# Performance work log

Measured on AMD Instinct MI355X. Metric: run time of the kernel, lower is better.

## Reference

```python
import jax, jax.numpy as jnp
import numpy as np

N, D = 8192, 32
SIGMA = 4.0
DAMPING = 0.5
MAX_ITER = 10
SHIFT_TOL = 1e-4


def _sqdist(a, b):
    # squared euclidean distances, (Na, Nb)
    sq = jnp.sum(a * a, axis=1)[:, None] + jnp.sum(b * b, axis=1)[None, :] - 2.0 * (a @ b.T)
    return jnp.maximum(sq, 0.0)


def setup_inputs() -> dict:
    key = jax.random.key(0)
    x = jax.random.normal(key, (N, D), dtype=jnp.float32)
    sigma = jnp.asarray(SIGMA, dtype=jnp.float32)  # learned scalar nn.Parameter
    return {"x": x, "sigma": sigma}


def _find_centroids(x, sigma):
    gamma = 1.0 / (2.0 * sigma ** 2)

    def body(carry, _):
        centroids, done = carry
        sq = _sqdist(x, centroids)              # (N, N); cdist(x,c)**2
        w = jnp.exp(-sq * gamma)                # gaussian kernel weights
        new_c = (w @ x) / jnp.sum(w, axis=1, keepdims=True)
        shift = jnp.linalg.norm(new_c - centroids, axis=1)
        # torch breaks BEFORE the damping update when max shift < tol
        done_new = done | (jnp.max(shift) < SHIFT_TOL)
        centroids = jnp.where(done_new, centroids,
                              DAMPING * centroids + (1.0 - DAMPING) * new_c)
        return (centroids, done_new), None

    (centroids, _), _ = jax.lax.scan(jax.remat(body), (x, jnp.asarray(False)), None, length=MAX_ITER)
    return centroids


def _nms_keep(x, centroids, threshold):
    n = centroids.shape[0]
    sq_pc = _sqdist(x, centroids)
    closest = jnp.argmin(sq_pc, axis=1)                      # (N,)
    scores = jnp.zeros((n,), jnp.int32).at[closest].add(1)   # counts per centroid
    sq_cc = _sqdist(centroids, centroids)
    overlap = (sq_cc < threshold ** 2) & ~jnp.eye(n, dtype=bool)
    order = jnp.argsort(-scores)                             # descending by score

    def body(keep, idx):
        active = keep[idx]
        keep2 = jnp.where(active, keep & ~overlap[idx], keep)
        keep2 = keep2.at[idx].set(jnp.where(active, scores[idx] > 0, keep2[idx]))
        return keep2, None

    keep, _ = jax.lax.scan(body, jnp.ones((n,), bool), order)
    return keep


def reference(x, sigma):
    centroids = _find_centroids(x, sigma)
    # threshold = sigma.item() in torch -> constant w.r.t. autodiff
    keep = _nms_keep(x, centroids, jax.lax.stop_gradient(sigma))
    # assignment over kept centroids only (dropped centroids get -inf cost -> 0 prob)
    cost = -jnp.sqrt(_sqdist(x, centroids) + 1e-12)
    cost = jnp.where(keep[None, :], cost, -jnp.inf)
    assignment = jax.nn.softmax(cost, axis=1)  # alpha == 1 branch
    return centroids, assignment, keep
```

## Files before the change

### kernel.cpp

```cpp
#include <hip/hip_runtime.h>
#include <math.h>

#define NPTS 8192
#define DIM 32
#define MAX_ITER 10
#define TOL 1e-4f
#define DAMP 0.5f
#define LOG2E 1.4426950408889634f

#define OFF_MSP   0u
#define OFF_CCUR  8650752u
#define OFF_CNEW  8912896u
#define OFF_NX    9175040u
#define OFF_NC    9183232u
#define OFF_PV    9191424u
#define OFF_PJ    9453568u
#define OFF_RKP   9715712u
#define OFF_MSH   9977856u
#define OFF_SCO   9977872u
#define OFF_ORD   9986064u

__global__ __launch_bounds__(256) void k_init(const float* __restrict__ x,
                                              float* __restrict__ c0,
                                              float* __restrict__ nx,
                                              float* __restrict__ nc,
                                              int* __restrict__ scores,
                                              unsigned int* __restrict__ msh) {
    int p = blockIdx.x * blockDim.x + threadIdx.x;
    const float4* xr = (const float4*)(x + (size_t)p * DIM);
    float4* cr = (float4*)(c0 + (size_t)p * DIM);
    float s = 0.f;
#pragma unroll
    for (int q = 0; q < 8; ++q) {
        float4 v = xr[q];
        cr[q] = v;
        s += v.x * v.x + v.y * v.y + v.z * v.z + v.w * v.w;
    }
    nx[p] = s;
    nc[p] = s;
    scores[p] = 0;
    if (blockIdx.x == 0 && threadIdx.x < 16) msh[threadIdx.x] = 0u;
}

__global__ __launch_bounds__(256, 2) void k_ms2(const float* __restrict__ x,
                                                const float* __restrict__ nx,
                                                const float* __restrict__ c,
                                                const float* __restrict__ nc,
                                                const float* __restrict__ sigma_p,
                                                float* __restrict__ P) {
    __shared__ float sc[256 * 32];
    __shared__ float sxx[128 * 32];
    __shared__ float snc[256];

    int t = threadIdx.x;
    int wv = __builtin_amdgcn_readfirstlane(t >> 6);
    int lane = t & 63;
    int it = (int)blockIdx.x >> 5, js = (int)blockIdx.x & 31;
    int i0 = it * 512 + wv * 128 + lane;
    int i1 = i0 + 64;
    int jb = js * 256;

    float sg = sigma_p[0];
    float ng2 = -LOG2E / (2.f * sg * sg);

    float xi0[DIM], xi1[DIM];
    {
        const float4* xr0 = (const float4*)(x + (size_t)i0 * DIM);
        const float4* xr1 = (const float4*)(x + (size_t)i1 * DIM);
#pragma unroll
        for (int q = 0; q < 8; ++q) {
            float4 a = xr0[q], b = xr1[q];
            xi0[4 * q] = a.x; xi0[4 * q + 1] = a.y; xi0[4 * q + 2] = a.z; xi0[4 * q + 3] = a.w;
            xi1[4 * q] = b.x; xi1[4 * q + 1] = b.y; xi1[4 * q + 2] = b.z; xi1[4 * q + 3] = b.w;
        }
    }
    float nx0 = nx[i0], nx1 = nx[i1];

    {
        const float4* srcc = (const float4*)(c + (size_t)jb * DIM);
        float4* dstc = (float4*)sc;
        for (int k = t; k < 2048; k += 256) dstc[k] = srcc[k];
        snc[t] = nc[jb + t];
        const float4* srcx = (const float4*)(x + (size_t)jb * DIM);
        float4* dstx = (float4*)sxx;
        for (int k = t; k < 1024; k += 256) dstx[k] = srcx[k];
    }
    __syncthreads();

    float acc0[DIM], acc1[DIM];
#pragma unroll
    for (int d = 0; d < DIM; ++d) { acc0[d] = 0.f; acc1[d] = 0.f; }
    float ws0 = 0.f, ws1 = 0.f;

    for (int half = 0; half < 2; ++half) {
        int jo = half * 128;
        for (int jj = 0; jj < 128; ++jj) {
            float w0, w1;
            {
                const float4* cr = (const float4*)(sc + (size_t)(jo + jj) * 32);
                float4 C[8];
#pragma unroll
                for (int q = 0; q < 8; ++q) C[q] = cr[q];
                float ncj = snc[jo + jj];
                float a0 = 0.f, a1 = 0.f, a2 = 0.f, a3 = 0.f;
                float b0 = 0.f, b1 = 0.f, b2 = 0.f, b3 = 0.f;
#pragma unroll
                for (int q = 0; q < 8; ++q) {
                    a0 = fmaf(xi0[4 * q + 0], C[q].x, a0);
                    a1 = fmaf(xi0[4 * q + 1], C[q].y, a1);
                    a2 = fmaf(xi0[4 * q + 2], C[q].z, a2);
                    a3 = fmaf(xi0[4 * q + 3], C[q].w, a3);
                    b0 = fmaf(xi1[4 * q + 0], C[q].x, b0);
                    b1 = fmaf(xi1[4 * q + 1], C[q].y, b1);
                    b2 = fmaf(xi1[4 * q + 2], C[q].z, b2);
                    b3 = fmaf(xi1[4 * q + 3], C[q].w, b3);
                }
                float sq0 = fmaxf(fmaf(-2.f, (a0 + a1) + (a2 + a3), nx0 + ncj), 0.f);
                float sq1 = fmaxf(fmaf(-2.f, (b0 + b1) + (b2 + b3), nx1 + ncj), 0.f);
                w0 = __builtin_amdgcn_exp2f(ng2 * sq0);
                w1 = __builtin_amdgcn_exp2f(ng2 * sq1);
            }
            ws0 += w0; ws1 += w1;
            {
                const float4* xr2 = (const float4*)(sxx + (size_t)jj * 32);
                float4 X[8];
#pragma unroll
                for (int q = 0; q < 8; ++q) X[q] = xr2[q];
#pragma unroll
                for (int q = 0; q < 8; ++q) {
                    acc0[4 * q + 0] = fmaf(w0, X[q].x, acc0[4 * q + 0]);
                    acc0[4 * q + 1] = fmaf(w0, X[q].y, acc0[4 * q + 1]);
                    acc0[4 * q + 2] = fmaf(w0, X[q].z, acc0[4 * q + 2]);
                    acc0[4 * q + 3] = fmaf(w0, X[q].w, acc0[4 * q + 3]);
                    acc1[4 * q + 0] = fmaf(w1, X[q].x, acc1[4 * q + 0]);
                    acc1[4 * q + 1] = fmaf(w1, X[q].y, acc1[4 * q + 1]);
                    acc1[4 * q + 2] = fmaf(w1, X[q].z, acc1[4 * q + 2]);
                    acc1[4 * q + 3] = fmaf(w1, X[q].w, acc1[4 * q + 3]);
                }
            }
        }
        if (half == 0) {
            __syncthreads();
            const float4* srcx = (const float4*)(x + (size_t)(jb + 128) * DIM);
            float4* dstx = (float4*)sxx;
            for (int k = t; k < 1024; k += 256) dstx[k] = srcx[k];
            __syncthreads();
        }
    }

    size_t base = ((size_t)js * 33) * NPTS + i0;
#pragma unroll
    for (int d = 0; d < DIM; ++d) {
        P[base + (size_t)d * NPTS] = acc0[d];
        P[base + (size_t)d * NPTS + 64] = acc1[d];
    }
    P[base + (size_t)32 * NPTS] = ws0;
    P[base + (size_t)32 * NPTS + 64] = ws1;
}

__global__ __launch_bounds__(256) void k_reduce(const float* __restrict__ P,
                                                const float* __restrict__ c_cur,
                                                float* __restrict__ c_new,
                                                unsigned int* __restrict__ maxshift) {
    int i = blockIdx.x * 256 + threadIdx.x;
    float tot[33];
#pragma unroll
    for (int d = 0; d < 33; ++d) tot[d] = 0.f;
    for (int js = 0; js < 32; ++js) {
        size_t base = ((size_t)js * 33) * NPTS + i;
#pragma unroll
        for (int d = 0; d < 33; ++d) tot[d] += P[base + (size_t)d * NPTS];
    }
    float ws = tot[32];
    float inv = __builtin_amdgcn_rcpf(ws);
    inv = inv * (2.f - ws * inv);
    const float* co = c_cur + (size_t)i * DIM;
    float sh2 = 0.f;
    float ncv[DIM];
#pragma unroll
    for (int d = 0; d < DIM; ++d) {
        float v = tot[d] * inv;
        ncv[d] = v;
        float df = v - co[d];
        sh2 = fmaf(df, df, sh2);
    }
    float4* dst = (float4*)(c_new + (size_t)i * DIM);
#pragma unroll
    for (int q = 0; q < 8; ++q)
        dst[q] = make_float4(ncv[4 * q], ncv[4 * q + 1], ncv[4 * q + 2], ncv[4 * q + 3]);
    atomicMax(maxshift, __float_as_uint(__builtin_amdgcn_sqrtf(sh2)));
}

__global__ __launch_bounds__(256) void k_update(float* __restrict__ c_cur,
                                                const float* __restrict__ c_new,
                                                float* __restrict__ nc,
                                                const unsigned int* __restrict__ maxshift) {
    if (__uint_as_float(*maxshift) < TOL) return;
    int i = blockIdx.x * 256 + threadIdx.x;
    float4* cc = (float4*)(c_cur + (size_t)i * DIM);
    const float4* cn = (const float4*)(c_new + (size_t)i * DIM);
    float s = 0.f;
#pragma unroll
    for (int q = 0; q < 8; ++q) {
        float4 a = cc[q], b = cn[q];
        float4 r = make_float4(DAMP * a.x + (1.f - DAMP) * b.x,
                               DAMP * a.y + (1.f - DAMP) * b.y,
                               DAMP * a.z + (1.f - DAMP) * b.z,
                               DAMP * a.w + (1.f - DAMP) * b.w);
        cc[q] = r;
        s += r.x * r.x + r.y * r.y + r.z * r.z + r.w * r.w;
    }
    nc[i] = s;
}

__global__ __launch_bounds__(256, 2) void k_scores2(const float* __restrict__ x,
                                                    const float* __restrict__ nx,
                                                    const float* __restrict__ c,
                                                    const float* __restrict__ nc,
                                                    float* __restrict__ pv,
                                                    int* __restrict__ pj) {
    __shared__ float sc[256 * 32];
    __shared__ float snc[256];
    int t = threadIdx.x;
    int wv = __builtin_amdgcn_readfirstlane(t >> 6);
    int lane = t & 63;
    int it = (int)blockIdx.x >> 5, js = (int)blockIdx.x & 31;
    int p0 = it * 512 + wv * 128 + lane;
    int p1 = p0 + 64;
    int jb = js * 256;

    float xi0[DIM], xi1[DIM];
    {
        const float4* xr0 = (const float4*)(x + (size_t)p0 * DIM);
        const float4* xr1 = (const float4*)(x + (size_t)p1 * DIM);
#pragma unroll
        for (int q = 0; q < 8; ++q) {
            float4 a = xr0[q], b = xr1[q];
            xi0[4 * q] = a.x; xi0[4 * q + 1] = a.y; xi0[4 * q + 2] = a.z; xi0[4 * q + 3] = a.w;
            xi1[4 * q] = b.x; xi1[4 * q + 1] = b.y; xi1[4 * q + 2] = b.z; xi1[4 * q + 3] = b.w;
        }
    }
    float nxp0 = nx[p0], nxp1 = nx[p1];

    {
        const float4* srcc = (const float4*)(c + (size_t)jb * DIM);
        float4* dstc = (float4*)sc;
        for (int k = t; k < 2048; k += 256) dstc[k] = srcc[k];
        snc[t] = nc[jb + t];
    }
    __syncthreads();

    float bv0 = INFINITY, bv1 = INFINITY;
    int bj0 = jb, bj1 = jb;
    for (int jj = 0; jj < 256; ++jj) {
        const float4* cr = (const float4*)(sc + (size_t)jj * 32);
        float4 C[8];
#pragma unroll
        for (int q = 0; q < 8; ++q) C[q] = cr[q];
        float ncj = snc[jj];
        float a0 = 0.f, a1 = 0.f, a2 = 0.f, a3 = 0.f;
        float b0 = 0.f, b1 = 0.f, b2 = 0.f, b3 = 0.f;
#pragma unroll
        for (int q = 0; q < 8; ++q) {
            a0 = fmaf(xi0[4 * q + 0], C[q].x, a0);
            a1 = fmaf(xi0[4 * q + 1], C[q].y, a1);
            a2 = fmaf(xi0[4 * q + 2], C[q].z, a2);
            a3 = fmaf(xi0[4 * q + 3], C[q].w, a3);
            b0 = fmaf(xi1[4 * q + 0], C[q].x, b0);
            b1 = fmaf(xi1[4 * q + 1], C[q].y, b1);
            b2 = fmaf(xi1[4 * q + 2], C[q].z, b2);
            b3 = fmaf(xi1[4 * q + 3], C[q].w, b3);
        }
        float sq0 = fmaxf(fmaf(-2.f, (a0 + a1) + (a2 + a3), nxp0 + ncj), 0.f);
        float sq1 = fmaxf(fmaf(-2.f, (b0 + b1) + (b2 + b3), nxp1 + ncj), 0.f);
        if (sq0 < bv0) { bv0 = sq0; bj0 = jb + jj; }
        if (sq1 < bv1) { bv1 = sq1; bj1 = jb + jj; }
    }
    pv[(size_t)js * NPTS + p0] = bv0;
    pj[(size_t)js * NPTS + p0] = bj0;
    pv[(size_t)js * NPTS + p1] = bv1;
    pj[(size_t)js * NPTS + p1] = bj1;
}

__global__ __launch_bounds__(256) void k_score_comb(const float* __restrict__ pv,
                                                    const int* __restrict__ pj,
                                                    int* __restrict__ scores) {
    int p = blockIdx.x * 256 + threadIdx.x;
    float bv = pv[p];
    int bj = pj[p];
    for (int js = 1; js < 32; ++js) {
        float v = pv[(size_t)js * NPTS + p];
        int j = pj[(size_t)js * NPTS + p];
        if (v < bv) { bv = v; bj = j; }
    }
    atomicAdd(&scores[bj], 1);
}

__global__ __launch_bounds__(256) void k_rank_part(const int* __restrict__ scores,
                                                   int* __restrict__ rkp) {
    int t = threadIdx.x;
    int wv = __builtin_amdgcn_readfirstlane(t >> 6);
    int lane = t & 63;
    int it = (int)blockIdx.x >> 5, js = (int)blockIdx.x & 31;
    int p = it * 256 + wv * 64 + lane;
    int sp = scores[p];
    int j0 = js * 256;
    int r = 0;
    for (int jj = 0; jj < 256; ++jj) {
        int sj = scores[j0 + jj];
        int j = j0 + jj;
        r += (sj > sp) || (sj == sp && j < p);
    }
    rkp[(size_t)js * NPTS + p] = r;
}

__global__ __launch_bounds__(256) void k_rank_comb(const int* __restrict__ rkp,
                                                   int* __restrict__ order) {
    int p = blockIdx.x * 256 + threadIdx.x;
    int r = 0;
    for (int js = 0; js < 32; ++js) r += rkp[(size_t)js * NPTS + p];
    order[r] = p;
}

__global__ __launch_bounds__(1024) void k_nms(const float* __restrict__ c,
                                              const int* __restrict__ order,
                                              const int* __restrict__ scores,
                                              const float* __restrict__ sigma_p,
                                              float* __restrict__ keep_out) {
    __shared__ int s_ord[NPTS];
    __shared__ unsigned char kp[NPTS];
    __shared__ int s_first[16];
    __shared__ int s_next;
    int t = threadIdx.x;
    for (int q = t; q < NPTS; q += 1024) { s_ord[q] = order[q]; kp[q] = 1; }
    __syncthreads();
    float sg = sigma_p[0];
    float thr2 = sg * sg;

    int k = 0;
    while (k < NPTS) {
        int cand = k + t;
        bool hit = (cand < NPTS) && (kp[s_ord[cand]] != 0);
        unsigned long long b = __ballot(hit);
        int wave = t >> 6;
        if ((t & 63) == 0)
            s_first[wave] = b ? (k + (wave << 6) + (__ffsll((unsigned long long)b) - 1))
                              : 0x7fffffff;
        __syncthreads();
        if (t == 0) {
            int mn = s_first[0];
            for (int w2 = 1; w2 < 16; ++w2) mn = min(mn, s_first[w2]);
            s_next = mn;
        }
        __syncthreads();
        int kf = s_next;
        if (kf == 0x7fffffff) { k += 1024; continue; }

        int idx = s_ord[kf];
        float ci[DIM];
        const float4* cr = (const float4*)(c + (size_t)idx * DIM);
#pragma unroll
        for (int q = 0; q < 8; ++q) {
            float4 v = cr[q];
            ci[4 * q] = v.x; ci[4 * q + 1] = v.y; ci[4 * q + 2] = v.z; ci[4 * q + 3] = v.w;
        }
#pragma unroll
        for (int m2 = 0; m2 < 8; ++m2) {
            int j = t + m2 * 1024;
            const float4* cj = (const float4*)(c + (size_t)j * DIM);
            float sq = 0.f;
#pragma unroll
            for (int q = 0; q < 8; ++q) {
                float4 v = cj[q];
                float e0 = v.x - ci[4 * q], e1 = v.y - ci[4 * q + 1];
                float e2 = v.z - ci[4 * q + 2], e3 = v.w - ci[4 * q + 3];
                sq += e0 * e0 + e1 * e1 + e2 * e2 + e3 * e3;
            }
            if (j != idx && sq < thr2) kp[j] = 0;
        }
        __syncthreads();
        if (t == 0) kp[idx] = (scores[idx] > 0) ? 1 : 0;
        __syncthreads();
        k = kf + 1;
    }
    __syncthreads();
    for (int q = t; q < NPTS; q += 1024) keep_out[q] = kp[q] ? 1.0f : 0.0f;
}

__global__ __launch_bounds__(256, 2) void k_apass1(const float* __restrict__ x,
                                                   const float* __restrict__ nx,
                                                   const float* __restrict__ c,
                                                   const float* __restrict__ nc,
                                                   const float* __restrict__ keepf,
                                                   float* __restrict__ ps) {
    __shared__ float sc[256 * 32];
    __shared__ float snc[256];
    __shared__ float skp[256];
    int t = threadIdx.x;
    int wv = __builtin_amdgcn_readfirstlane(t >> 6);
    int lane = t & 63;
    int it = (int)blockIdx.x >> 5, js = (int)blockIdx.x & 31;
    int p0 = it * 512 + wv * 128 + lane;
    int p1 = p0 + 64;
    int jb = js * 256;

    float xi0[DIM], xi1[DIM];
    {
        const float4* xr0 = (const float4*)(x + (size_t)p0 * DIM);
        const float4* xr1 = (const float4*)(x + (size_t)p1 * DIM);
#pragma unroll
        for (int q = 0; q < 8; ++q) {
            float4 a = xr0[q], b = xr1[q];
            xi0[4 * q] = a.x; xi0[4 * q + 1] = a.y; xi0[4 * q + 2] = a.z; xi0[4 * q + 3] = a.w;
            xi1[4 * q] = b.x; xi1[4 * q + 1] = b.y; xi1[4 * q + 2] = b.z; xi1[4 * q + 3] = b.w;
        }
    }
    float nxp0 = nx[p0], nxp1 = nx[p1];

    {
        const float4* srcc = (const float4*)(c + (size_t)jb * DIM);
        float4* dstc = (float4*)sc;
        for (int k = t; k < 2048; k += 256) dstc[k] = srcc[k];
        snc[t] = nc[jb + t];
        skp[t] = (keepf[jb + t] > 0.5f) ? 0.f : -1e38f;
    }
    __syncthreads();

    float S0 = 0.f, S1 = 0.f;
    for (int jj = 0; jj < 256; ++jj) {
        const float4* cr = (const float4*)(sc + (size_t)jj * 32);
        float4 C[8];
#pragma unroll
        for (int q = 0; q < 8; ++q) C[q] = cr[q];
        float ncj = snc[jj];
        float kadd = skp[jj];
        float a0 = 0.f, a1 = 0.f, a2 = 0.f, a3 = 0.f;
        float b0 = 0.f, b1 = 0.f, b2 = 0.f, b3 = 0.f;
#pragma unroll
        for (int q = 0; q < 8; ++q) {
            a0 = fmaf(xi0[4 * q + 0], C[q].x, a0);
            a1 = fmaf(xi0[4 * q + 1], C[q].y, a1);
            a2 = fmaf(xi0[4 * q + 2], C[q].z, a2);
            a3 = fmaf(xi0[4 * q + 3], C[q].w, a3);
            b0 = fmaf(xi1[4 * q + 0], C[q].x, b0);
            b1 = fmaf(xi1[4 * q + 1], C[q].y, b1);
            b2 = fmaf(xi1[4 * q + 2], C[q].z, b2);
            b3 = fmaf(xi1[4 * q + 3], C[q].w, b3);
        }
        float sq0 = fmaxf(fmaf(-2.f, (a0 + a1) + (a2 + a3), nxp0 + ncj), 0.f);
        float sq1 = fmaxf(fmaf(-2.f, (b0 + b1) + (b2 + b3), nxp1 + ncj), 0.f);
        float r0 = __builtin_amdgcn_sqrtf(sq0 + 1e-12f);
        float r1 = __builtin_amdgcn_sqrtf(sq1 + 1e-12f);
        S0 += __builtin_amdgcn_exp2f(fmaf(r0, -LOG2E, kadd));
        S1 += __builtin_amdgcn_exp2f(fmaf(r1, -LOG2E, kadd));
    }
    ps[(size_t)js * NPTS + p0] = S0;
    ps[(size_t)js * NPTS + p1] = S1;
}

__global__ __launch_bounds__(256, 4) void k_apass2(const float* __restrict__ x,
                                                   const float* __restrict__ c,
                                                   const float* __restrict__ keepf,
                                                   const float* __restrict__ ps,
                                                   float* __restrict__ A) {
    __shared__ float sx[128 * 36];
    __shared__ float snx[128];
    __shared__ float sscale[128];
    __shared__ float spart[256];
    int t = threadIdx.x;
    int wv = __builtin_amdgcn_readfirstlane(t >> 6);
    int lane = t & 63;
    int pt = (int)blockIdx.x >> 5, jt = (int)blockIdx.x & 31;
    int p0 = pt * 128, j0 = jt * 256;

    {
        const float4* src = (const float4*)(x + (size_t)p0 * DIM) + t * 4;
        int row = t >> 1, colh = (t & 1) * 16;
        float4* dst = (float4*)(sx + row * 36 + colh);
        float s = 0.f;
#pragma unroll
        for (int q = 0; q < 4; ++q) {
            float4 v = src[q];
            dst[q] = v;
            s += v.x * v.x + v.y * v.y + v.z * v.z + v.w * v.w;
        }
        spart[t] = s;
    }
    __syncthreads();
    if (t < 128) {
        snx[t] = spart[2 * t] + spart[2 * t + 1];
        float SS = 0.f;
        for (int js = 0; js < 32; ++js) SS += ps[(size_t)js * NPTS + p0 + t];
        sscale[t] = 1.f / SS;
    }

    int j = j0 + wv * 64 + lane;
    float cj[DIM];
    float ncj = 0.f;
    {
        const float4* cr = (const float4*)(c + (size_t)j * DIM);
#pragma unroll
        for (int q = 0; q < 8; ++q) {
            float4 v = cr[q];
            cj[4 * q] = v.x; cj[4 * q + 1] = v.y; cj[4 * q + 2] = v.z; cj[4 * q + 3] = v.w;
            ncj += v.x * v.x + v.y * v.y + v.z * v.z + v.w * v.w;
        }
    }
    float kadd = (keepf[j] > 0.5f) ? 0.f : -1e38f;
    __syncthreads();

    for (int pp = 0; pp < 128; ++pp) {
        const float4* xs = (const float4*)(sx + pp * 36);
        float d0 = 0.f, d1 = 0.f, d2 = 0.f, d3 = 0.f;
#pragma unroll
        for (int q = 0; q < 8; ++q) {
            float4 v = xs[q];
            d0 = fmaf(cj[4 * q + 0], v.x, d0);
            d1 = fmaf(cj[4 * q + 1], v.y, d1);
            d2 = fmaf(cj[4 * q + 2], v.z, d2);
            d3 = fmaf(cj[4 * q + 3], v.w, d3);
        }
        float sq = fmaxf(fmaf(-2.f, (d0 + d1) + (d2 + d3), snx[pp] + ncj), 0.f);
        float rt = __builtin_amdgcn_sqrtf(sq + 1e-12f);
        float tt = fmaf(rt, -LOG2E, kadd);
        A[(size_t)(p0 + pp) * NPTS + j] = __builtin_amdgcn_exp2f(tt) * sscale[pp];
    }
}

extern "C" void kernel_launch(void* const* d_in, const int* in_sizes, int n_in,
                              void* d_out, int out_size, void* d_ws, size_t ws_size,
                              hipStream_t stream) {
    const float* x = (const float*)d_in[0];
    const float* sigma = (const float*)d_in[1];

    float* out = (float*)d_out;
    float* OUT_C = out;
    float* A = out + (size_t)NPTS * DIM;
    float* OUT_K = A + (size_t)NPTS * NPTS;

    float* msP = A + OFF_MSP;
    float* c_cur = A + OFF_CCUR;
    float* c_new = A + OFF_CNEW;
    float* nx = A + OFF_NX;
    float* nc = A + OFF_NC;
    float* pv = A + OFF_PV;
    int* pj = (int*)(A + OFF_PJ);
    int* rkp = (int*)(A + OFF_RKP);
    unsigned int* msh = (unsigned int*)(A + OFF_MSH);
    int* scores = (int*)(A + OFF_SCO);
    int* order = (int*)(A + OFF_ORD);
    float* ps = (float*)d_ws;

    k_init<<<NPTS / 256, 256, 0, stream>>>(x, c_cur, nx, nc, scores, msh);
    for (int itr = 0; itr < MAX_ITER; ++itr) {
        k_ms2<<<512, 256, 0, stream>>>(x, nx, c_cur, nc, sigma, msP);
        k_reduce<<<NPTS / 256, 256, 0, stream>>>(msP, c_cur, c_new, msh + itr);
        k_update<<<NPTS / 256, 256, 0, stream>>>(c_cur, c_new, nc, msh + itr);
    }
    hipMemcpyAsync(OUT_C, c_cur, (size_t)NPTS * DIM * sizeof(float),
                   hipMemcpyDeviceToDevice, stream);

    k_scores2<<<512, 256, 0, stream>>>(x, nx, OUT_C, nc, pv, pj);
    k_score_comb<<<NPTS / 256, 256, 0, stream>>>(pv, pj, scores);
    k_rank_part<<<1024, 256, 0, stream>>>(scores, rkp);
    k_rank_comb<<<NPTS / 256, 256, 0, stream>>>(rkp, order);
    k_nms<<<1, 1024, 0, stream>>>(OUT_C, order, scores, sigma, OUT_K);

    k_apass1<<<512, 256, 0, stream>>>(x, nx, OUT_C, nc, OUT_K, ps);
    k_apass2<<<2048, 256, 0, stream>>>(x, OUT_C, OUT_K, ps, A);
}
```

Measured before the change: 1.987 ms.

## Split mean-shift column tiles finer, parallelize reduction, widen assignment tiles

The mean-shift partial kernel now covers 128 centroid columns per block instead of 256. That doubles the grid to 1024 blocks, halves shared memory per block, and removes the mid-loop reload and barriers. The reduction kernel splits the 64 partial slices across four wave groups and combines them in shared memory, so it runs 128 blocks instead of 32. The assignment kernel computes two columns per thread on half as many blocks, and several inner loops read shared memory directly rather than staging a row in registers. The cost is a partial buffer twice as large to write and read each iteration, plus changed occupancy hints.

```diff
diff --git a/kernel.cpp b/kernel.cpp
--- a/kernel.cpp
+++ b/kernel.cpp
@@ -9,16 +9,16 @@
 #define LOG2E 1.4426950408889634f
 
 #define OFF_MSP   0u
-#define OFF_CCUR  8650752u
-#define OFF_CNEW  8912896u
-#define OFF_NX    9175040u
-#define OFF_NC    9183232u
-#define OFF_PV    9191424u
-#define OFF_PJ    9453568u
-#define OFF_RKP   9715712u
-#define OFF_MSH   9977856u
-#define OFF_SCO   9977872u
-#define OFF_ORD   9986064u
+#define OFF_CCUR  17301504u
+#define OFF_CNEW  17563648u
+#define OFF_NX    17825792u
+#define OFF_NC    17833984u
+#define OFF_PV    17842176u
+#define OFF_PJ    18366464u
+#define OFF_RKP   18890752u
+#define OFF_MSH   19152896u
+#define OFF_SCO   19152912u
+#define OFF_ORD   19161104u
 
 __global__ __launch_bounds__(256) void k_init(const float* __restrict__ x,
                                               float* __restrict__ c0,
@@ -42,23 +42,25 @@
     if (blockIdx.x == 0 && threadIdx.x < 16) msh[threadIdx.x] = 0u;
 }
 
-__global__ __launch_bounds__(256, 2) void k_ms2(const float* __restrict__ x,
-                                                const float* __restrict__ nx,
-                                                const float* __restrict__ c,
-                                                const float* __restrict__ nc,
-                                                const float* __restrict__ sigma_p,
-                                                float* __restrict__ P) {
-    __shared__ float sc[256 * 32];
+__global__ __launch_bounds__(256)
+__attribute__((amdgpu_waves_per_eu(2, 4)))
+void k_ms2(const float* __restrict__ x,
+           const float* __restrict__ nx,
+           const float* __restrict__ c,
+           const float* __restrict__ nc,
+           const float* __restrict__ sigma_p,
+           float* __restrict__ P) {
+    __shared__ float sc[128 * 32];
     __shared__ float sxx[128 * 32];
-    __shared__ float snc[256];
+    __shared__ float snc[128];
 
     int t = threadIdx.x;
     int wv = __builtin_amdgcn_readfirstlane(t >> 6);
     int lane = t & 63;
-    int it = (int)blockIdx.x >> 5, js = (int)blockIdx.x & 31;
+    int it = (int)blockIdx.x >> 6, js = (int)blockIdx.x & 63;
     int i0 = it * 512 + wv * 128 + lane;
     int i1 = i0 + 64;
-    int jb = js * 256;
+    int jb = js * 128;
 
     float sg = sigma_p[0];
     float ng2 = -LOG2E / (2.f * sg * sg);
@@ -78,12 +80,11 @@
 
     {
         const float4* srcc = (const float4*)(c + (size_t)jb * DIM);
+        const float4* srcx = (const float4*)(x + (size_t)jb * DIM);
         float4* dstc = (float4*)sc;
-        for (int k = t; k < 2048; k += 256) dstc[k] = srcc[k];
-        snc[t] = nc[jb + t];
-        const float4* srcx = (const float4*)(x + (size_t)jb * DIM);
         float4* dstx = (float4*)sxx;
-        for (int k = t; k < 1024; k += 256) dstx[k] = srcx[k];
+        for (int k = t; k < 1024; k += 256) { dstc[k] = srcc[k]; dstx[k] = srcx[k]; }
+        if (t < 128) snc[t] = nc[jb + t];
     }
     __syncthreads();
 
@@ -92,59 +93,42 @@
     for (int d = 0; d < DIM; ++d) { acc0[d] = 0.f; acc1[d] = 0.f; }
     float ws0 = 0.f, ws1 = 0.f;
 
-    for (int half = 0; half < 2; ++half) {
-        int jo = half * 128;
-        for (int jj = 0; jj < 128; ++jj) {
-            float w0, w1;
-            {
-                const float4* cr = (const float4*)(sc + (size_t)(jo + jj) * 32);
-                float4 C[8];
-#pragma unroll
-                for (int q = 0; q < 8; ++q) C[q] = cr[q];
-                float ncj = snc[jo + jj];
-                float a0 = 0.f, a1 = 0.f, a2 = 0.f, a3 = 0.f;
-                float b0 = 0.f, b1 = 0.f, b2 = 0.f, b3 = 0.f;
-#pragma unroll
-                for (int q = 0; q < 8; ++q) {
-                    a0 = fmaf(xi0[4 * q + 0], C[q].x, a0);
-                    a1 = fmaf(xi0[4 * q + 1], C[q].y, a1);
-                    a2 = fmaf(xi0[4 * q + 2], C[q].z, a2);
-                    a3 = fmaf(xi0[4 * q + 3], C[q].w, a3);
-                    b0 = fmaf(xi1[4 * q + 0], C[q].x, b0);
-                    b1 = fmaf(xi1[4 * q + 1], C[q].y, b1);
-                    b2 = fmaf(xi1[4 * q + 2], C[q].z, b2);
-                    b3 = fmaf(xi1[4 * q + 3], C[q].w, b3);
-                }
-                float sq0 = fmaxf(fmaf(-2.f, (a0 + a1) + (a2 + a3), nx0 + ncj), 0.f);
-                float sq1 = fmaxf(fmaf(-2.f, (b0 + b1) + (b2 + b3), nx1 + ncj), 0.f);
-                w0 = __builtin_amdgcn_exp2f(ng2 * sq0);
-                w1 = __builtin_amdgcn_exp2f(ng2 * sq1);
+    for (int jj = 0; jj < 128; ++jj) {
+        int rb = jj * 32;
+        float w0, w1;
+        {
+            float a0 = 0.f, a1 = 0.f, a2 = 0.f, a3 = 0.f;
+            float b0 = 0.f, b1 = 0.f, b2 = 0.f, b3 = 0.f;
+#pragma unroll
+            for (int q = 0; q < 8; ++q) {
+                float4 cv = *(const float4*)(sc + rb + 4 * q);
+                a0 = fmaf(xi0[4 * q + 0], cv.x, a0);
+                a1 = fmaf(xi0[4 * q + 1], cv.y, a1);
+                a2 = fmaf(xi0[4 * q + 2], cv.z, a2);
+                a3 = fmaf(xi0[4 * q + 3], cv.w, a3);
+                b0 = fmaf(xi1[4 * q + 0], cv.x, b0);
+                b1 = fmaf(xi1[4 * q + 1], cv.y, b1);
+                b2 = fmaf(xi1[4 * q + 2], cv.z, b2);
+                b3 = fmaf(xi1[4 * q + 3], cv.w, b3);
             }
-            ws0 += w0; ws1 += w1;
-            {
-                const float4* xr2 = (const float4*)(sxx + (size_t)jj * 32);
-                float4 X[8];
-#pragma unroll
-                for (int q = 0; q < 8; ++q) X[q] = xr2[q];
-#pragma unroll
-                for (int q = 0; q < 8; ++q) {
-                    acc0[4 * q + 0] = fmaf(w0, X[q].x, acc0[4 * q + 0]);
-                    acc0[4 * q + 1] = fmaf(w0, X[q].y, acc0[4 * q + 1]);
-                    acc0[4 * q + 2] = fmaf(w0, X[q].z, acc0[4 * q + 2]);
-                    acc0[4 * q + 3] = fmaf(w0, X[q].w, acc0[4 * q + 3]);
-                    acc1[4 * q + 0] = fmaf(w1, X[q].x, acc1[4 * q + 0]);
-                    acc1[4 * q + 1] = fmaf(w1, X[q].y, acc1[4 * q + 1]);
-                    acc1[4 * q + 2] = fmaf(w1, X[q].z, acc1[4 * q + 2]);
-                    acc1[4 * q + 3] = fmaf(w1, X[q].w, acc1[4 * q + 3]);
-                }
-            }
-        }
-        if (half == 0) {
-            __syncthreads();
-            const float4* srcx = (const float4*)(x + (size_t)(jb + 128) * DIM);
-            float4* dstx = (float4*)sxx;
-            for (int k = t; k < 1024; k += 256) dstx[k] = srcx[k];
-            __syncthreads();
+            float ncj = snc[jj];
+            float sq0 = fmaxf(fmaf(-2.f, (a0 + a1) + (a2 + a3), nx0 + ncj), 0.f);
+            float sq1 = fmaxf(fmaf(-2.f, (b0 + b1) + (b2 + b3), nx1 + ncj), 0.f);
+            w0 = __builtin_amdgcn_exp2f(ng2 * sq0);
+            w1 = __builtin_amdgcn_exp2f(ng2 * sq1);
+        }
+        ws0 += w0; ws1 += w1;
+#pragma unroll
+        for (int q = 0; q < 8; ++q) {
+            float4 xv = *(const float4*)(sxx + rb + 4 * q);
+            acc0[4 * q + 0] = fmaf(w0, xv.x, acc0[4 * q + 0]);
+            acc0[4 * q + 1] = fmaf(w0, xv.y, acc0[4 * q + 1]);
+            acc0[4 * q + 2] = fmaf(w0, xv.z, acc0[4 * q + 2]);
+            acc0[4 * q + 3] = fmaf(w0, xv.w, acc0[4 * q + 3]);
+            acc1[4 * q + 0] = fmaf(w1, xv.x, acc1[4 * q + 0]);
+            acc1[4 * q + 1] = fmaf(w1, xv.y, acc1[4 * q + 1]);
+            acc1[4 * q + 2] = fmaf(w1, xv.z, acc1[4 * q + 2]);
+            acc1[4 * q + 3] = fmaf(w1, xv.w, acc1[4 * q + 3]);
         }
     }
 
@@ -162,33 +146,46 @@
                                                 const float* __restrict__ c_cur,
                                                 float* __restrict__ c_new,
                                                 unsigned int* __restrict__ maxshift) {
-    int i = blockIdx.x * 256 + threadIdx.x;
+    __shared__ float red[256][33];
+    int t = threadIdx.x;
+    int pl = t & 63, qs = t >> 6;
+    int i = blockIdx.x * 64 + pl;
     float tot[33];
 #pragma unroll
     for (int d = 0; d < 33; ++d) tot[d] = 0.f;
-    for (int js = 0; js < 32; ++js) {
+    for (int js = qs * 16; js < qs * 16 + 16; ++js) {
         size_t base = ((size_t)js * 33) * NPTS + i;
 #pragma unroll
         for (int d = 0; d < 33; ++d) tot[d] += P[base + (size_t)d * NPTS];
     }
-    float ws = tot[32];
-    float inv = __builtin_amdgcn_rcpf(ws);
-    inv = inv * (2.f - ws * inv);
-    const float* co = c_cur + (size_t)i * DIM;
-    float sh2 = 0.f;
-    float ncv[DIM];
-#pragma unroll
-    for (int d = 0; d < DIM; ++d) {
-        float v = tot[d] * inv;
-        ncv[d] = v;
-        float df = v - co[d];
-        sh2 = fmaf(df, df, sh2);
-    }
-    float4* dst = (float4*)(c_new + (size_t)i * DIM);
-#pragma unroll
-    for (int q = 0; q < 8; ++q)
-        dst[q] = make_float4(ncv[4 * q], ncv[4 * q + 1], ncv[4 * q + 2], ncv[4 * q + 3]);
-    atomicMax(maxshift, __float_as_uint(__builtin_amdgcn_sqrtf(sh2)));
+#pragma unroll
+    for (int d = 0; d < 33; ++d) red[t][d] = tot[d];
+    __syncthreads();
+    if (t < 64) {
+        int ii = blockIdx.x * 64 + t;
+        float tt[33];
+#pragma unroll
+        for (int d = 0; d < 33; ++d)
+            tt[d] = (red[t][d] + red[t + 64][d]) + (red[t + 128][d] + red[t + 192][d]);
+        float ws = tt[32];
+        float inv = __builtin_amdgcn_rcpf(ws);
+        inv = inv * (2.f - ws * inv);
+        const float* co = c_cur + (size_t)ii * DIM;
+        float sh2 = 0.f;
+        float ncv[DIM];
+#pragma unroll
+        for (int d = 0; d < DIM; ++d) {
+            float v = tt[d] * inv;
+            ncv[d] = v;
+            float df = v - co[d];
+            sh2 = fmaf(df, df, sh2);
+        }
+        float4* dst = (float4*)(c_new + (size_t)ii * DIM);
+#pragma unroll
+        for (int q = 0; q < 8; ++q)
+            dst[q] = make_float4(ncv[4 * q], ncv[4 * q + 1], ncv[4 * q + 2], ncv[4 * q + 3]);
+        atomicMax(maxshift, __float_as_uint(__builtin_amdgcn_sqrtf(sh2)));
+    }
 }
 
 __global__ __launch_bounds__(256) void k_update(float* __restrict__ c_cur,
@@ -253,24 +250,22 @@
     float bv0 = INFINITY, bv1 = INFINITY;
     int bj0 = jb, bj1 = jb;
     for (int jj = 0; jj < 256; ++jj) {
-        const float4* cr = (const float4*)(sc + (size_t)jj * 32);
-        float4 C[8];
-#pragma unroll
-        for (int q = 0; q < 8; ++q) C[q] = cr[q];
-        float ncj = snc[jj];
+        int rb = jj * 32;
         float a0 = 0.f, a1 = 0.f, a2 = 0.f, a3 = 0.f;
         float b0 = 0.f, b1 = 0.f, b2 = 0.f, b3 = 0.f;
 #pragma unroll
         for (int q = 0; q < 8; ++q) {
-            a0 = fmaf(xi0[4 * q + 0], C[q].x, a0);
-            a1 = fmaf(xi0[4 * q + 1], C[q].y, a1);
-            a2 = fmaf(xi0[4 * q + 2], C[q].z, a2);
-            a3 = fmaf(xi0[4 * q + 3], C[q].w, a3);
-            b0 = fmaf(xi1[4 * q + 0], C[q].x, b0);
-            b1 = fmaf(xi1[4 * q + 1], C[q].y, b1);
-            b2 = fmaf(xi1[4 * q + 2], C[q].z, b2);
-            b3 = fmaf(xi1[4 * q + 3], C[q].w, b3);
-        }
+            float4 cv = *(const float4*)(sc + rb + 4 * q);
+            a0 = fmaf(xi0[4 * q + 0], cv.x, a0);
+            a1 = fmaf(xi0[4 * q + 1], cv.y, a1);
+            a2 = fmaf(xi0[4 * q + 2], cv.z, a2);
+            a3 = fmaf(xi0[4 * q + 3], cv.w, a3);
+            b0 = fmaf(xi1[4 * q + 0], cv.x, b0);
+            b1 = fmaf(xi1[4 * q + 1], cv.y, b1);
+            b2 = fmaf(xi1[4 * q + 2], cv.z, b2);
+            b3 = fmaf(xi1[4 * q + 3], cv.w, b3);
+        }
+        float ncj = snc[jj];
         float sq0 = fmaxf(fmaf(-2.f, (a0 + a1) + (a2 + a3), nxp0 + ncj), 0.f);
         float sq1 = fmaxf(fmaf(-2.f, (b0 + b1) + (b2 + b3), nxp1 + ncj), 0.f);
         if (sq0 < bv0) { bv0 = sq0; bj0 = jb + jj; }
@@ -428,25 +423,23 @@
 
     float S0 = 0.f, S1 = 0.f;
     for (int jj = 0; jj < 256; ++jj) {
-        const float4* cr = (const float4*)(sc + (size_t)jj * 32);
-        float4 C[8];
-#pragma unroll
-        for (int q = 0; q < 8; ++q) C[q] = cr[q];
+        int rb = jj * 32;
+        float a0 = 0.f, a1 = 0.f, a2 = 0.f, a3 = 0.f;
+        float b0 = 0.f, b1 = 0.f, b2 = 0.f, b3 = 0.f;
+#pragma unroll
+        for (int q = 0; q < 8; ++q) {
+            float4 cv = *(const float4*)(sc + rb + 4 * q);
+            a0 = fmaf(xi0[4 * q + 0], cv.x, a0);
+            a1 = fmaf(xi0[4 * q + 1], cv.y, a1);
+            a2 = fmaf(xi0[4 * q + 2], cv.z, a2);
+            a3 = fmaf(xi0[4 * q + 3], cv.w, a3);
+            b0 = fmaf(xi1[4 * q + 0], cv.x, b0);
+            b1 = fmaf(xi1[4 * q + 1], cv.y, b1);
+            b2 = fmaf(xi1[4 * q + 2], cv.z, b2);
+            b3 = fmaf(xi1[4 * q + 3], cv.w, b3);
+        }
         float ncj = snc[jj];
         float kadd = skp[jj];
-        float a0 = 0.f, a1 = 0.f, a2 = 0.f, a3 = 0.f;
-        float b0 = 0.f, b1 = 0.f, b2 = 0.f, b3 = 0.f;
-#pragma unroll
-        for (int q = 0; q < 8; ++q) {
-            a0 = fmaf(xi0[4 * q + 0], C[q].x, a0);
-            a1 = fmaf(xi0[4 * q + 1], C[q].y, a1);
-            a2 = fmaf(xi0[4 * q + 2], C[q].z, a2);
-            a3 = fmaf(xi0[4 * q + 3], C[q].w, a3);
-            b0 = fmaf(xi1[4 * q + 0], C[q].x, b0);
-            b1 = fmaf(xi1[4 * q + 1], C[q].y, b1);
-            b2 = fmaf(xi1[4 * q + 2], C[q].z, b2);
-            b3 = fmaf(xi1[4 * q + 3], C[q].w, b3);
-        }
         float sq0 = fmaxf(fmaf(-2.f, (a0 + a1) + (a2 + a3), nxp0 + ncj), 0.f);
         float sq1 = fmaxf(fmaf(-2.f, (b0 + b1) + (b2 + b3), nxp1 + ncj), 0.f);
         float r0 = __builtin_amdgcn_sqrtf(sq0 + 1e-12f);
@@ -458,11 +451,13 @@
     ps[(size_t)js * NPTS + p1] = S1;
 }
 
-__global__ __launch_bounds__(256, 4) void k_apass2(const float* __restrict__ x,
-                                                   const float* __restrict__ c,
-                                                   const float* __restrict__ keepf,
-                                                   const float* __restrict__ ps,
-                                                   float* __restrict__ A) {
+__global__ __launch_bounds__(256)
+__attribute__((amdgpu_waves_per_eu(3, 4)))
+void k_apass2(const float* __restrict__ x,
+              const float* __restrict__ c,
+              const float* __restrict__ keepf,
+              const float* __restrict__ ps,
+              float* __restrict__ A) {
     __shared__ float sx[128 * 36];
     __shared__ float snx[128];
     __shared__ float sscale[128];
@@ -470,8 +465,8 @@
     int t = threadIdx.x;
     int wv = __builtin_amdgcn_readfirstlane(t >> 6);
     int lane = t & 63;
-    int pt = (int)blockIdx.x >> 5, jt = (int)blockIdx.x & 31;
-    int p0 = pt * 128, j0 = jt * 256;
+    int pt = (int)blockIdx.x >> 4, jt = (int)blockIdx.x & 15;
+    int p0 = pt * 128, j0 = jt * 512;
 
     {
         const float4* src = (const float4*)(x + (size_t)p0 * DIM) + t * 4;
@@ -494,36 +489,52 @@
         sscale[t] = 1.f / SS;
     }
 
-    int j = j0 + wv * 64 + lane;
-    float cj[DIM];
-    float ncj = 0.f;
-    {
-        const float4* cr = (const float4*)(c + (size_t)j * DIM);
-#pragma unroll
-        for (int q = 0; q < 8; ++q) {
-            float4 v = cr[q];
-            cj[4 * q] = v.x; cj[4 * q + 1] = v.y; cj[4 * q + 2] = v.z; cj[4 * q + 3] = v.w;
-            ncj += v.x * v.x + v.y * v.y + v.z * v.z + v.w * v.w;
-        }
-    }
-    float kadd = (keepf[j] > 0.5f) ? 0.f : -1e38f;
+    int ja = j0 + wv * 64 + lane;
+    int jbx = ja + 256;
+    float cj0[DIM], cj1[DIM];
+    float nc0 = 0.f, nc1 = 0.f;
+    {
+        const float4* cra = (const float4*)(c + (size_t)ja * DIM);
+        const float4* crb = (const float4*)(c + (size_t)jbx * DIM);
+#pragma unroll
+        for (int q = 0; q < 8; ++q) {
+            float4 va = cra[q], vb = crb[q];
+            cj0[4 * q] = va.x; cj0[4 * q + 1] = va.y; cj0[4 * q + 2] = va.z; cj0[4 * q + 3] = va.w;
+            cj1[4 * q] = vb.x; cj1[4 * q + 1] = vb.y; cj1[4 * q + 2] = vb.z; cj1[4 * q + 3] = vb.w;
+            nc0 += va.x * va.x + va.y * va.y + va.z * va.z + va.w * va.w;
+            nc1 += vb.x * vb.x + vb.y * vb.y + vb.z * vb.z + vb.w * vb.w;
+        }
+    }
+    float kadd0 = (keepf[ja] > 0.5f) ? 0.f : -1e38f;
+    float kadd1 = (keepf[jbx] > 0.5f) ? 0.f : -1e38f;
     __syncthreads();
 
     for (int pp = 0; pp < 128; ++pp) {
-        const float4* xs = (const float4*)(sx + pp * 36);
+        int rb = pp * 36;
         float d0 = 0.f, d1 = 0.f, d2 = 0.f, d3 = 0.f;
-#pragma unroll
-        for (int q = 0; q < 8; ++q) {
-            float4 v = xs[q];
-            d0 = fmaf(cj[4 * q + 0], v.x, d0);
-            d1 = fmaf(cj[4 * q + 1], v.y, d1);
-            d2 = fmaf(cj[4 * q + 2], v.z, d2);
-            d3 = fmaf(cj[4 * q + 3], v.w, d3);
-        }
-        float sq = fmaxf(fmaf(-2.f, (d0 + d1) + (d2 + d3), snx[pp] + ncj), 0.f);
-        float rt = __builtin_amdgcn_sqrtf(sq + 1e-12f);
-        float tt = fmaf(rt, -LOG2E, kadd);
-        A[(size_t)(p0 + pp) * NPTS + j] = __builtin_amdgcn_exp2f(tt) * sscale[pp];
+        float e0 = 0.f, e1 = 0.f, e2 = 0.f, e3 = 0.f;
+#pragma unroll
+        for (int q = 0; q < 8; ++q) {
+            float4 v = *(const float4*)(sx + rb + 4 * q);
+            d0 = fmaf(cj0[4 * q + 0], v.x, d0);
+            d1 = fmaf(cj0[4 * q + 1], v.y, d1);
+            d2 = fmaf(cj0[4 * q + 2], v.z, d2);
+            d3 = fmaf(cj0[4 * q + 3], v.w, d3);
+            e0 = fmaf(cj1[4 * q + 0], v.x, e0);
+            e1 = fmaf(cj1[4 * q + 1], v.y, e1);
+            e2 = fmaf(cj1[4 * q + 2], v.z, e2);
+            e3 = fmaf(cj1[4 * q + 3], v.w, e3);
+        }
+        float nxp = snx[pp], scl = sscale[pp];
+        float sqa = fmaxf(fmaf(-2.f, (d0 + d1) + (d2 + d3), nxp + nc0), 0.f);
+        float sqb = fmaxf(fmaf(-2.f, (e0 + e1) + (e2 + e3), nxp + nc1), 0.f);
+        float ra = __builtin_amdgcn_sqrtf(sqa + 1e-12f);
+        float rbq = __builtin_amdgcn_sqrtf(sqb + 1e-12f);
+        float ta = fmaf(ra, -LOG2E, kadd0);
+        float tb = fmaf(rbq, -LOG2E, kadd1);
+        float* rowp = A + (size_t)(p0 + pp) * NPTS;
+        rowp[ja] = __builtin_amdgcn_exp2f(ta) * scl;
+        rowp[jbx] = __builtin_amdgcn_exp2f(tb) * scl;
     }
 }
 
@@ -553,8 +564,8 @@
 
     k_init<<<NPTS / 256, 256, 0, stream>>>(x, c_cur, nx, nc, scores, msh);
     for (int itr = 0; itr < MAX_ITER; ++itr) {
-        k_ms2<<<512, 256, 0, stream>>>(x, nx, c_cur, nc, sigma, msP);
-        k_reduce<<<NPTS / 256, 256, 0, stream>>>(msP, c_cur, c_new, msh + itr);
+        k_ms2<<<1024, 256, 0, stream>>>(x, nx, c_cur, nc, sigma, msP);
+        k_reduce<<<NPTS / 64, 256, 0, stream>>>(msP, c_cur, c_new, msh + itr);
         k_update<<<NPTS / 256, 256, 0, stream>>>(c_cur, c_new, nc, msh + itr);
     }
     hipMemcpyAsync(OUT_C, c_cur, (size_t)NPTS * DIM * sizeof(float),
@@ -567,5 +578,5 @@
     k_nms<<<1, 1024, 0, stream>>>(OUT_C, order, scores, sigma, OUT_K);
 
     k_apass1<<<512, 256, 0, stream>>>(x, nx, OUT_C, nc, OUT_K, ps);
-    k_apass2<<<2048, 256, 0, stream>>>(x, OUT_C, OUT_K, ps, A);
-}
+    k_apass2<<<1024, 256, 0, stream>>>(x, OUT_C, OUT_K, ps, A);
+}
```

After: 1.992 ms. About the same (+0.2%).
